# Performance work log

Hardware: AMD Instinct MI355X
Metric: run time of the kernel (lower is better)

## Reference

```python
import jax, jax.numpy as jnp
import numpy as np

EPS = 1e-5  # torch BatchNorm default eps


def _bn_relu(x, g, b, relu):
    # Training-mode BatchNorm1d over (N, C, L): stats over axes (0, 2).
    m = jnp.mean(x, axis=(0, 2), keepdims=True)
    v = jnp.var(x, axis=(0, 2), keepdims=True)
    y = (x - m) * jax.lax.rsqrt(v + EPS) * g[None, :, None] + b[None, :, None]
    return jax.nn.relu(y) if relu else y


def setup_inputs() -> dict:
    key = jax.random.key(0)
    k0, k1, k2 = jax.random.split(key, 3)
    N, C, H = 256, 512, 64  # batch, channels (inplanes==planes), spatial positions (mask_channel)
    x = jax.random.normal(k0, (N, C, H), dtype=jnp.float32)
    # LocallyConnected2d weights: torch shape (1, out, in, H, 1, k^2=1) -> (out, in, H)
    w1 = jax.random.normal(k1, (C, C, H), dtype=jnp.float32) * 0.02
    w2 = jax.random.normal(k2, (C, C, H), dtype=jnp.float32) * 0.02
    g1 = jnp.ones((C,), jnp.float32)
    b1 = jnp.zeros((C,), jnp.float32)
    g2 = jnp.ones((C,), jnp.float32)
    b2 = jnp.zeros((C,), jnp.float32)
    return {"x": x, "w1": w1, "g1": g1, "b1": b1, "w2": w2, "g2": g2, "b2": b2}


def reference(x, w1, g1, b1, w2, g2, b2):
    # conv1: locally-connected 1x1 -> per-position matmul over channels
    out = jnp.einsum('nch,och->noh', x, w1)          # (N, C, H)
    out = _bn_relu(out, g1, b1, relu=True)
    # conv2
    out = jnp.einsum('nch,och->noh', out, w2)
    out = _bn_relu(out, g2, b2, relu=False)
    # residual add (downsample is None) + final relu
    return jax.nn.relu(out + x)
```

## Files before the change

### kernel.cpp

```cpp
#include <hip/hip_runtime.h>
#include <stdint.h>

typedef float  f32x4  __attribute__((ext_vector_type(4)));
typedef __bf16 bf16x8 __attribute__((ext_vector_type(8)));
typedef __bf16 bf16x4 __attribute__((ext_vector_type(4)));

#define N_ 256
#define C_ 512
#define H_ 64
#define RS_ 32768

__device__ __forceinline__ uint32_t pack_bf16x2(float a, float b) {
  const uint16_t ua = __builtin_bit_cast(uint16_t, (__bf16)a);
  const uint16_t ub = __builtin_bit_cast(uint16_t, (__bf16)b);
  return (uint32_t)ua | ((uint32_t)ub << 16);
}

__global__ __launch_bounds__(256) void k_prep(const float* __restrict__ x,
                                              const float* __restrict__ w1,
                                              const float* __restrict__ w2,
                                              __bf16* __restrict__ xT,
                                              __bf16* __restrict__ w1T,
                                              __bf16* __restrict__ w2T,
                                              float* __restrict__ stats) {
  __shared__ uint32_t tile[128][32];
  const int t  = threadIdx.x;
  const int by = blockIdx.y;
  if (by == 0 && blockIdx.x == 0) {
#pragma unroll
    for (int i = 0; i < 8; ++i) stats[i * 256 + t] = 0.f;
  }
  const float* src;
  __bf16* dst;
  int p;
  if (by < 256)      { src = x;  dst = xT;  p = by; }
  else if (by < 768) { src = w1; dst = w1T; p = by - 256; }
  else               { src = w2; dst = w2T; p = by - 768; }
  const int ch0 = blockIdx.x * 128;
  const float* sbase = src + ((size_t)p * 512 + ch0) * 64;

#pragma unroll
  for (int j = 0; j < 8; ++j) {
    const int fidx = j * 256 + t;
    const int c = fidx >> 4, hq = fidx & 15;
    const float4 v = *reinterpret_cast<const float4*>(sbase + c * 64 + hq * 4);
    const int wp = (hq + (c >> 3)) & 15;
    uint2 pk;
    pk.x = pack_bf16x2(v.x, v.y);
    pk.y = pack_bf16x2(v.z, v.w);
    *reinterpret_cast<uint2*>(&tile[c][wp * 2]) = pk;
  }
  __syncthreads();

  __bf16* dbase = dst + (size_t)p * RS_ + ch0;
#pragma unroll
  for (int j = 0; j < 4; ++j) {
    const int ci = j * 256 + t;
    const int cb = ci & 15, h = ci >> 4;
    const int hm = h >> 1;
    const bool odd = (h & 1) != 0;
    uint32_t W[8];
#pragma unroll
    for (int i = 0; i < 8; ++i) {
      const int c = cb * 8 + i;
      const int w = (((hm >> 1) + cb) & 15) * 2 + (hm & 1);
      W[i] = tile[c][w];
    }
    uint4 o;
    uint32_t* op = reinterpret_cast<uint32_t*>(&o);
#pragma unroll
    for (int k = 0; k < 4; ++k) {
      const uint32_t wa = W[2 * k], wb = W[2 * k + 1];
      op[k] = odd ? ((wa >> 16) | (wb & 0xFFFF0000u))
                  : ((wa & 0xFFFFu) | (wb << 16));
    }
    *reinterpret_cast<uint4*>(dbase + (size_t)h * 512 + cb * 8) = o;
  }
}

template <bool BN_A>
__global__ __launch_bounds__(256, 2) void k_gemm(
    const __bf16* __restrict__ A,
    const __bf16* __restrict__ B,
    __bf16* __restrict__ Co,
    const float* __restrict__ sum_in, const float* __restrict__ sq_in,
    const float* __restrict__ g, const float* __restrict__ bb,
    float* __restrict__ sum_out, float* __restrict__ sq_out) {
  const int wkid = (blockIdx.x & 7) * 64 + (blockIdx.x >> 3);
  const int h  = wkid >> 3;
  const int tm = (wkid >> 2) & 1, tn = wkid & 3;
  const int m0 = tm * 128, n0 = tn * 128;
  const __bf16* Ah = A + (size_t)m0 * RS_ + (size_t)h * C_;
  const __bf16* Bh = B + (size_t)n0 * RS_ + (size_t)h * C_;
  __shared__ __bf16 As[2][128 * 64];
  __shared__ __bf16 Bs[2][128 * 64];
  __shared__ float a_lds[512], c_lds[512];
  const int tid  = threadIdx.x;
  const int lane = tid & 63, wid = tid >> 6;
  const int wr = wid >> 1, wc = wid & 1;
  const int lrow8 = lane >> 3;
  const int swz   = (lane & 7) ^ lrow8;

  if (BN_A) {
#pragma unroll
    for (int ch = tid; ch < 512; ch += 256) {
      const float m    = sum_in[ch] * (1.f / 16384.f);
      const float var  = fmaxf(0.f, sq_in[ch] * (1.f / 16384.f) - m * m);
      const float aa   = g[ch] * rsqrtf(var + 1e-5f);
      a_lds[ch] = aa;
      c_lds[ch] = bb[ch] - m * aa;
    }
    __syncthreads();
  }

  auto stage_b = [&](int buf, int kt) {
#pragma unroll
    for (int i = 0; i < 4; ++i) {
      const int rbase = wid * 32 + i * 8;
      const __bf16* gb = Bh + (size_t)(rbase + lrow8) * RS_ + kt * 64 + swz * 8;
      __builtin_amdgcn_global_load_lds(
          (const __attribute__((address_space(1))) void*)gb,
          (__attribute__((address_space(3))) void*)(&Bs[buf][rbase * 64]), 16, 0, 0);
    }
  };
  auto stage_a = [&](int buf, int kt) {
#pragma unroll
    for (int i = 0; i < 4; ++i) {
      const int rbase = wid * 32 + i * 8;
      const __bf16* ga = Ah + (size_t)(rbase + lrow8) * RS_ + kt * 64 + swz * 8;
      __builtin_amdgcn_global_load_lds(
          (const __attribute__((address_space(1))) void*)ga,
          (__attribute__((address_space(3))) void*)(&As[buf][rbase * 64]), 16, 0, 0);
    }
  };
  const int lr32 = tid >> 3, cch = tid & 7;
  auto load_a = [&](bf16x8* v, int kt) {
#pragma unroll
    for (int i = 0; i < 4; ++i)
      v[i] = *reinterpret_cast<const bf16x8*>(
          Ah + (size_t)(i * 32 + lr32) * RS_ + kt * 64 + cch * 8);
  };
  auto bn_write = [&](const bf16x8* v, int buf, int kt) {
    const int cg = kt * 64 + cch * 8;
    const f32x4 s0 = *reinterpret_cast<const f32x4*>(&a_lds[cg]);
    const f32x4 s1 = *reinterpret_cast<const f32x4*>(&a_lds[cg + 4]);
    const f32x4 h0 = *reinterpret_cast<const f32x4*>(&c_lds[cg]);
    const f32x4 h1 = *reinterpret_cast<const f32x4*>(&c_lds[cg + 4]);
#pragma unroll
    for (int i = 0; i < 4; ++i) {
      const int row = i * 32 + lr32;
      bf16x8 y;
#pragma unroll
      for (int e = 0; e < 4; ++e) {
        y[e]     = (__bf16)fmaxf(0.f, fmaf((float)v[i][e],     s0[e], h0[e]));
        y[e + 4] = (__bf16)fmaxf(0.f, fmaf((float)v[i][e + 4], s1[e], h1[e]));
      }
      const int boff = row * 128 + ((cch * 16) ^ ((row & 7) << 4));
      *reinterpret_cast<bf16x8*>(reinterpret_cast<char*>(&As[buf][0]) + boff) = y;
    }
  };

  f32x4 acc[4][4] = {};
  const int fr = lane & 15, kc = lane >> 4;
  auto compute = [&](int buf) {
#pragma unroll
    for (int kk = 0; kk < 2; ++kk) {
      bf16x8 af[4], bfq[4];
#pragma unroll
      for (int mf = 0; mf < 4; ++mf) {
        const int row  = wr * 64 + mf * 16 + fr;
        const int boff = row * 128 + ((kk * 64 + kc * 16) ^ ((row & 7) << 4));
        af[mf] = *reinterpret_cast<const bf16x8*>(
            reinterpret_cast<const char*>(&As[buf][0]) + boff);
      }
#pragma unroll
      for (int nf = 0; nf < 4; ++nf) {
        const int row  = wc * 64 + nf * 16 + fr;
        const int boff = row * 128 + ((kk * 64 + kc * 16) ^ ((row & 7) << 4));
        bfq[nf] = *reinterpret_cast<const bf16x8*>(
            reinterpret_cast<const char*>(&Bs[buf][0]) + boff);
      }
#pragma unroll
      for (int mf = 0; mf < 4; ++mf)
#pragma unroll
        for (int nf = 0; nf < 4; ++nf)
          acc[mf][nf] = __builtin_amdgcn_mfma_f32_16x16x32_bf16(af[mf], bfq[nf], acc[mf][nf], 0, 0, 0);
    }
  };

  if (BN_A) {
    bf16x8 v0[4];
    load_a(v0, 0);
    bn_write(v0, 0, 0);
  } else {
    stage_a(0, 0);
  }
  stage_b(0, 0);
  __syncthreads();

  int buf = 0;
  for (int kt = 0; kt < 8; ++kt) {
    bf16x8 vn[4];
    if (kt < 7) {
      stage_b(buf ^ 1, kt + 1);
      if (!BN_A) stage_a(buf ^ 1, kt + 1);
      else       load_a(vn, kt + 1);
    }
    compute(buf);
    if (BN_A && kt < 7) bn_write(vn, buf ^ 1, kt + 1);
    __syncthreads();
    buf ^= 1;
  }

  const int rq = (lane >> 4) * 4;
#pragma unroll
  for (int nf = 0; nf < 4; ++nf) {
    const int oc = n0 + wc * 64 + nf * 16 + fr;
    float s = 0.f, s2 = 0.f;
#pragma unroll
    for (int mf = 0; mf < 4; ++mf) {
      const int rb = m0 + wr * 64 + mf * 16 + rq;
      f32x4 v = acc[mf][nf];
#pragma unroll
      for (int j = 0; j < 4; ++j) {
        const float f = v[j];
        Co[(size_t)(rb + j) * RS_ + (size_t)h * C_ + oc] = (__bf16)f;
        s += f;
        s2 += f * f;
      }
    }
    s  += __shfl_xor(s, 16);  s  += __shfl_xor(s, 32);
    s2 += __shfl_xor(s2, 16); s2 += __shfl_xor(s2, 32);
    if (lane < 16) {
      atomicAdd(&sum_out[oc], s);
      atomicAdd(&sq_out[oc], s2);
    }
  }
}

__global__ __launch_bounds__(256) void k_finalize(const __bf16* __restrict__ t2,
                                                  const float* __restrict__ x,
                                                  const float* __restrict__ sum2,
                                                  const float* __restrict__ sq2,
                                                  const float* __restrict__ g2,
                                                  const float* __restrict__ b2,
                                                  float* __restrict__ out) {
  __shared__ float tile[64][65];
  __shared__ float a2s[64], c2s[64];
  const int n  = blockIdx.y;
  const int o0 = blockIdx.x * 64;
  const int t  = threadIdx.x;
  if (t < 64) {
    const int o = o0 + t;
    const float m    = sum2[o] * (1.f / 16384.f);
    const float var  = fmaxf(0.f, sq2[o] * (1.f / 16384.f) - m * m);
    const float a    = g2[o] * rsqrtf(var + 1e-5f);
    a2s[t] = a;
    c2s[t] = b2[o] - m * a;
  }
  const __bf16* tb = t2 + (size_t)n * RS_ + o0;
#pragma unroll
  for (int j = 0; j < 4; ++j) {
    const int hh = j * 16 + (t >> 4);
    const int ol = (t & 15) * 4;
    const bf16x4 v = *reinterpret_cast<const bf16x4*>(tb + (size_t)hh * 512 + ol);
#pragma unroll
    for (int e = 0; e < 4; ++e) tile[hh][ol + e] = (float)v[e];
  }
  __syncthreads();
  const int ol = t >> 2;
  const int hb = (t & 3) * 16;
  const int o  = o0 + ol;
  const float a = a2s[ol], c = c2s[ol];
  const float4* xp = reinterpret_cast<const float4*>(x + ((size_t)n * C_ + o) * H_ + hb);
  float4* op = reinterpret_cast<float4*>(out + ((size_t)n * C_ + o) * H_ + hb);
#pragma unroll
  for (int i4 = 0; i4 < 4; ++i4) {
    const float4 xv = xp[i4];
    float4 r;
    r.x = fmaxf(0.f, fmaf(a, tile[hb + i4 * 4 + 0][ol], c) + xv.x);
    r.y = fmaxf(0.f, fmaf(a, tile[hb + i4 * 4 + 1][ol], c) + xv.y);
    r.z = fmaxf(0.f, fmaf(a, tile[hb + i4 * 4 + 2][ol], c) + xv.z);
    r.w = fmaxf(0.f, fmaf(a, tile[hb + i4 * 4 + 3][ol], c) + xv.w);
    op[i4] = r;
  }
}

extern "C" void kernel_launch(void* const* d_in, const int* in_sizes, int n_in,
                              void* d_out, int out_size, void* d_ws, size_t ws_size,
                              hipStream_t stream) {
  const float* x  = (const float*)d_in[0];
  const float* w1 = (const float*)d_in[1];
  const float* g1 = (const float*)d_in[2];
  const float* b1 = (const float*)d_in[3];
  const float* w2 = (const float*)d_in[4];
  const float* g2 = (const float*)d_in[5];
  const float* b2 = (const float*)d_in[6];
  float* out = (float*)d_out;

  char* ws = (char*)d_ws;
  float* stats = (float*)ws;
  float* sum1 = stats,        *sq1 = stats + 512;
  float* sum2 = stats + 1024, *sq2 = stats + 1536;
  const size_t MB = (size_t)1 << 20;
  __bf16* xT  = (__bf16*)(ws + 64 * 1024);
  __bf16* w1T = (__bf16*)(ws + 64 * 1024 + 16 * MB);
  __bf16* w2T = (__bf16*)(ws + 64 * 1024 + 48 * MB);
  __bf16* t1T = (__bf16*)(ws + 64 * 1024 + 80 * MB);
  __bf16* t2T = (__bf16*)(ws + 64 * 1024 + 96 * MB);

  k_prep<<<dim3(4, 1280), 256, 0, stream>>>(x, w1, w2, xT, w1T, w2T, stats);

  k_gemm<false><<<512, 256, 0, stream>>>(xT, w1T, t1T, nullptr, nullptr,
                                         nullptr, nullptr, sum1, sq1);
  k_gemm<true><<<512, 256, 0, stream>>>(t1T, w2T, t2T, sum1, sq1, g1, b1,
                                        sum2, sq2);

  k_finalize<<<dim3(8, 256), 256, 0, stream>>>(t2T, x, sum2, sq2, g2, b2, out);
}
```

Baseline: 105.2 us.

## Overlap w2 conversion with GEMM1 and software-pipeline the transpose-prep tiles

Conversion and transposition of w2 to bf16 moves out of the standalone prep kernel into the GEMM1 launch, where half of the blocks do the w2 prep and the other half do GEMM1 tiles. The goal is to hide the memory-bound w2 conversion behind the compute-bound GEMM. Each prep block now handles four positions with double-buffered LDS, so global loads for the next tile overlap the shuffle and store of the current one. The costs are more LDS per prep block, a larger fixed smem footprint in the fused kernel, and possible imbalance between the two kinds of block.

Result: no change. 107.2 us (+1.9%).

```diff
diff --git a/kernel.cpp b/kernel.cpp
--- a/kernel.cpp
+++ b/kernel.cpp
@@ -16,86 +16,89 @@
   return (uint32_t)ua | ((uint32_t)ub << 16);
 }
 
-__global__ __launch_bounds__(256) void k_prep(const float* __restrict__ x,
-                                              const float* __restrict__ w1,
-                                              const float* __restrict__ w2,
-                                              __bf16* __restrict__ xT,
-                                              __bf16* __restrict__ w1T,
-                                              __bf16* __restrict__ w2T,
-                                              float* __restrict__ stats) {
-  __shared__ uint32_t tile[128][32];
-  const int t  = threadIdx.x;
-  const int by = blockIdx.y;
-  if (by == 0 && blockIdx.x == 0) {
-#pragma unroll
-    for (int i = 0; i < 8; ++i) stats[i * 256 + t] = 0.f;
-  }
-  const float* src;
-  __bf16* dst;
-  int p;
-  if (by < 256)      { src = x;  dst = xT;  p = by; }
-  else if (by < 768) { src = w1; dst = w1T; p = by - 256; }
-  else               { src = w2; dst = w2T; p = by - 768; }
-  const int ch0 = blockIdx.x * 128;
-  const float* sbase = src + ((size_t)p * 512 + ch0) * 64;
-
-#pragma unroll
-  for (int j = 0; j < 8; ++j) {
-    const int fidx = j * 256 + t;
-    const int c = fidx >> 4, hq = fidx & 15;
-    const float4 v = *reinterpret_cast<const float4*>(sbase + c * 64 + hq * 4);
-    const int wp = (hq + (c >> 3)) & 15;
-    uint2 pk;
-    pk.x = pack_bf16x2(v.x, v.y);
-    pk.y = pack_bf16x2(v.z, v.w);
-    *reinterpret_cast<uint2*>(&tile[c][wp * 2]) = pk;
-  }
+__device__ __forceinline__ void prep_tile4(const float* __restrict__ src,
+                                           __bf16* __restrict__ dst,
+                                           int pg, int qc, int t,
+                                           uint32_t* lds) {
+  uint32_t* bufs[2] = { lds, lds + 128 * 32 };
+  const int ch0 = qc * 128;
+  float4 v[8];
+  auto load_regs = [&](int p) {
+    const float* sb = src + ((size_t)p * 512 + ch0) * 64;
+#pragma unroll
+    for (int j = 0; j < 8; ++j) {
+      const int fidx = j * 256 + t;
+      const int c = fidx >> 4, hq = fidx & 15;
+      v[j] = *reinterpret_cast<const float4*>(sb + c * 64 + hq * 4);
+    }
+  };
+  auto lds_write = [&](uint32_t* b) {
+#pragma unroll
+    for (int j = 0; j < 8; ++j) {
+      const int fidx = j * 256 + t;
+      const int c = fidx >> 4, hq = fidx & 15;
+      const int wp = (hq + (c >> 3)) & 15;
+      uint2 pk;
+      pk.x = pack_bf16x2(v[j].x, v[j].y);
+      pk.y = pack_bf16x2(v[j].z, v[j].w);
+      *reinterpret_cast<uint2*>(&b[c * 32 + wp * 2]) = pk;
+    }
+  };
+  auto phase2 = [&](const uint32_t* bsrc, int p) {
+    __bf16* db = dst + (size_t)p * RS_ + ch0;
+#pragma unroll
+    for (int j = 0; j < 4; ++j) {
+      const int ci = j * 256 + t;
+      const int cb = ci & 15, h = ci >> 4;
+      const int hm = h >> 1;
+      const bool odd = (h & 1) != 0;
+      uint32_t W[8];
+#pragma unroll
+      for (int i = 0; i < 8; ++i) {
+        const int c = cb * 8 + i;
+        const int w = (((hm >> 1) + cb) & 15) * 2 + (hm & 1);
+        W[i] = bsrc[c * 32 + w];
+      }
+      uint4 o;
+      uint32_t* op = reinterpret_cast<uint32_t*>(&o);
+#pragma unroll
+      for (int k = 0; k < 4; ++k) {
+        const uint32_t wa = W[2 * k], wb = W[2 * k + 1];
+        op[k] = odd ? ((wa >> 16) | (wb & 0xFFFF0000u))
+                    : ((wa & 0xFFFFu) | (wb << 16));
+      }
+      *reinterpret_cast<uint4*>(db + (size_t)h * 512 + cb * 8) = o;
+    }
+  };
+
+  const int p0 = pg * 4;
+  load_regs(p0);
+  lds_write(bufs[0]);
   __syncthreads();
-
-  __bf16* dbase = dst + (size_t)p * RS_ + ch0;
-#pragma unroll
-  for (int j = 0; j < 4; ++j) {
-    const int ci = j * 256 + t;
-    const int cb = ci & 15, h = ci >> 4;
-    const int hm = h >> 1;
-    const bool odd = (h & 1) != 0;
-    uint32_t W[8];
-#pragma unroll
-    for (int i = 0; i < 8; ++i) {
-      const int c = cb * 8 + i;
-      const int w = (((hm >> 1) + cb) & 15) * 2 + (hm & 1);
-      W[i] = tile[c][w];
-    }
-    uint4 o;
-    uint32_t* op = reinterpret_cast<uint32_t*>(&o);
-#pragma unroll
-    for (int k = 0; k < 4; ++k) {
-      const uint32_t wa = W[2 * k], wb = W[2 * k + 1];
-      op[k] = odd ? ((wa >> 16) | (wb & 0xFFFF0000u))
-                  : ((wa & 0xFFFFu) | (wb << 16));
-    }
-    *reinterpret_cast<uint4*>(dbase + (size_t)h * 512 + cb * 8) = o;
+#pragma unroll
+  for (int i = 0; i < 4; ++i) {
+    if (i < 3) load_regs(p0 + i + 1);
+    phase2(bufs[i & 1], p0 + i);
+    if (i < 3) lds_write(bufs[(i + 1) & 1]);
+    __syncthreads();
   }
 }
 
 template <bool BN_A>
-__global__ __launch_bounds__(256, 2) void k_gemm(
-    const __bf16* __restrict__ A,
-    const __bf16* __restrict__ B,
+__device__ __forceinline__ void gemm_body(
+    const __bf16* __restrict__ A, const __bf16* __restrict__ B,
     __bf16* __restrict__ Co,
     const float* __restrict__ sum_in, const float* __restrict__ sq_in,
     const float* __restrict__ g, const float* __restrict__ bb,
-    float* __restrict__ sum_out, float* __restrict__ sq_out) {
-  const int wkid = (blockIdx.x & 7) * 64 + (blockIdx.x >> 3);
+    float* __restrict__ sum_out, float* __restrict__ sq_out,
+    int gblk, int tid, __bf16* AsB, __bf16* BsB,
+    float* a_lds, float* c_lds) {
+  const int wkid = (gblk & 7) * 64 + (gblk >> 3);
   const int h  = wkid >> 3;
   const int tm = (wkid >> 2) & 1, tn = wkid & 3;
   const int m0 = tm * 128, n0 = tn * 128;
   const __bf16* Ah = A + (size_t)m0 * RS_ + (size_t)h * C_;
   const __bf16* Bh = B + (size_t)n0 * RS_ + (size_t)h * C_;
-  __shared__ __bf16 As[2][128 * 64];
-  __shared__ __bf16 Bs[2][128 * 64];
-  __shared__ float a_lds[512], c_lds[512];
-  const int tid  = threadIdx.x;
   const int lane = tid & 63, wid = tid >> 6;
   const int wr = wid >> 1, wc = wid & 1;
   const int lrow8 = lane >> 3;
@@ -120,7 +123,8 @@
       const __bf16* gb = Bh + (size_t)(rbase + lrow8) * RS_ + kt * 64 + swz * 8;
       __builtin_amdgcn_global_load_lds(
           (const __attribute__((address_space(1))) void*)gb,
-          (__attribute__((address_space(3))) void*)(&Bs[buf][rbase * 64]), 16, 0, 0);
+          (__attribute__((address_space(3))) void*)(BsB + buf * 8192 + rbase * 64),
+          16, 0, 0);
     }
   };
   auto stage_a = [&](int buf, int kt) {
@@ -130,7 +134,8 @@
       const __bf16* ga = Ah + (size_t)(rbase + lrow8) * RS_ + kt * 64 + swz * 8;
       __builtin_amdgcn_global_load_lds(
           (const __attribute__((address_space(1))) void*)ga,
-          (__attribute__((address_space(3))) void*)(&As[buf][rbase * 64]), 16, 0, 0);
+          (__attribute__((address_space(3))) void*)(AsB + buf * 8192 + rbase * 64),
+          16, 0, 0);
     }
   };
   const int lr32 = tid >> 3, cch = tid & 7;
@@ -156,7 +161,7 @@
         y[e + 4] = (__bf16)fmaxf(0.f, fmaf((float)v[i][e + 4], s1[e], h1[e]));
       }
       const int boff = row * 128 + ((cch * 16) ^ ((row & 7) << 4));
-      *reinterpret_cast<bf16x8*>(reinterpret_cast<char*>(&As[buf][0]) + boff) = y;
+      *reinterpret_cast<bf16x8*>(reinterpret_cast<char*>(AsB + buf * 8192) + boff) = y;
     }
   };
 
@@ -171,14 +176,14 @@
         const int row  = wr * 64 + mf * 16 + fr;
         const int boff = row * 128 + ((kk * 64 + kc * 16) ^ ((row & 7) << 4));
         af[mf] = *reinterpret_cast<const bf16x8*>(
-            reinterpret_cast<const char*>(&As[buf][0]) + boff);
+            reinterpret_cast<const char*>(AsB + buf * 8192) + boff);
       }
 #pragma unroll
       for (int nf = 0; nf < 4; ++nf) {
         const int row  = wc * 64 + nf * 16 + fr;
         const int boff = row * 128 + ((kk * 64 + kc * 16) ^ ((row & 7) << 4));
         bfq[nf] = *reinterpret_cast<const bf16x8*>(
-            reinterpret_cast<const char*>(&Bs[buf][0]) + boff);
+            reinterpret_cast<const char*>(BsB + buf * 8192) + boff);
       }
 #pragma unroll
       for (int mf = 0; mf < 4; ++mf)
@@ -236,6 +241,55 @@
       atomicAdd(&sq_out[oc], s2);
     }
   }
+}
+
+__global__ __launch_bounds__(256) void k_prep_xw1(const float* __restrict__ x,
+                                                  const float* __restrict__ w1,
+                                                  __bf16* __restrict__ xT,
+                                                  __bf16* __restrict__ w1T,
+                                                  float* __restrict__ stats) {
+  __shared__ uint32_t lds[2 * 128 * 32];
+  const int bid = blockIdx.x, t = threadIdx.x;
+  if (bid == 0) {
+#pragma unroll
+    for (int i = 0; i < 8; ++i) stats[i * 256 + t] = 0.f;
+  }
+  const bool isx = bid < 256;
+  const float* src = isx ? x : w1;
+  __bf16* dst = isx ? xT : w1T;
+  const int b = isx ? bid : bid - 256;
+  prep_tile4(src, dst, b >> 2, b & 3, t, lds);
+}
+
+__global__ __launch_bounds__(256, 2) void k_gemm1_prepw2(
+    const __bf16* __restrict__ xT, const __bf16* __restrict__ w1T,
+    __bf16* __restrict__ t1T,
+    float* __restrict__ sum1, float* __restrict__ sq1,
+    const float* __restrict__ w2, __bf16* __restrict__ w2T) {
+  __shared__ __align__(16) char smem[65536];
+  const int bid = blockIdx.x, t = threadIdx.x;
+  const int sub = (bid >> 4) * 8 + (bid & 7);
+  if ((bid & 15) < 8) {
+    gemm_body<false>(xT, w1T, t1T, nullptr, nullptr, nullptr, nullptr,
+                     sum1, sq1, sub, t,
+                     (__bf16*)smem, (__bf16*)(smem + 32768), nullptr, nullptr);
+  } else {
+    prep_tile4(w2, w2T, sub >> 2, sub & 3, t, (uint32_t*)smem);
+  }
+}
+
+__global__ __launch_bounds__(256, 2) void k_gemm2(
+    const __bf16* __restrict__ t1T, const __bf16* __restrict__ w2T,
+    __bf16* __restrict__ t2T,
+    const float* __restrict__ sum1, const float* __restrict__ sq1,
+    const float* __restrict__ g1, const float* __restrict__ b1,
+    float* __restrict__ sum2, float* __restrict__ sq2) {
+  __shared__ __bf16 As[2][8192];
+  __shared__ __bf16 Bs[2][8192];
+  __shared__ float a_lds[512], c_lds[512];
+  gemm_body<true>(t1T, w2T, t2T, sum1, sq1, g1, b1, sum2, sq2,
+                  (int)blockIdx.x, (int)threadIdx.x,
+                  &As[0][0], &Bs[0][0], a_lds, c_lds);
 }
 
 __global__ __launch_bounds__(256) void k_finalize(const __bf16* __restrict__ t2,
@@ -309,12 +363,8 @@
   __bf16* t1T = (__bf16*)(ws + 64 * 1024 + 80 * MB);
   __bf16* t2T = (__bf16*)(ws + 64 * 1024 + 96 * MB);
 
-  k_prep<<<dim3(4, 1280), 256, 0, stream>>>(x, w1, w2, xT, w1T, w2T, stats);
-
-  k_gemm<false><<<512, 256, 0, stream>>>(xT, w1T, t1T, nullptr, nullptr,
-                                         nullptr, nullptr, sum1, sq1);
-  k_gemm<true><<<512, 256, 0, stream>>>(t1T, w2T, t2T, sum1, sq1, g1, b1,
-                                        sum2, sq2);
-
+  k_prep_xw1<<<768, 256, 0, stream>>>(x, w1, xT, w1T, stats);
+  k_gemm1_prepw2<<<1024, 256, 0, stream>>>(xT, w1T, t1T, sum1, sq1, w2, w2T);
+  k_gemm2<<<512, 256, 0, stream>>>(t1T, w2T, t2T, sum1, sq1, g1, b1, sum2, sq2);
   k_finalize<<<dim3(8, 256), 256, 0, stream>>>(t2T, x, sum2, sq2, g2, b2, out);
 }
```
